# Kernel optimization log

Measured on AMD Instinct MI355X. Metric: run time of the kernel, lower is better.

## Reference

```python
import jax, jax.numpy as jnp
import numpy as np

B, TD, SD, H = 512, 2048, 768, 128


def setup_inputs() -> dict:
    key = jax.random.key(0)
    ks = jax.random.split(key, 12)
    s = lambda k, shape, fan_in: jax.random.normal(k, shape, jnp.float32) * (1.0 / np.sqrt(fan_in))
    return {
        "teacher_features": jax.random.normal(ks[0], (B, TD), jnp.float32),
        "student_features": jax.random.normal(ks[1], (B, SD), jnp.float32),
        # Linear weights stored [in, out] (transposed vs torch) so y = x @ W + b
        "Wt": s(ks[2], (TD, H), TD), "bt": jnp.zeros((H,), jnp.float32),
        "Ws": s(ks[3], (SD, H), SD), "bs": jnp.zeros((H,), jnp.float32),
        "W1": s(ks[4], (2 * H, H), 2 * H), "b1": jnp.zeros((H,), jnp.float32),
        "W2": s(ks[5], (H, 1), H), "b2": jnp.zeros((1,), jnp.float32),
    }


def reference(teacher_features, student_features, Wt, bt, Ws, bs, W1, b1, W2, b2):
    def compute_relations(f):
        b, h = f.shape
        # pairwise concat [f_i, f_j] -> [B, B, 2H]
        pair = jnp.concatenate(
            [jnp.broadcast_to(f[:, None, :], (b, b, h)),
             jnp.broadcast_to(f[None, :, :], (b, b, h))], axis=-1)
        hdn = jax.nn.relu(jnp.einsum('ijk,kh->ijh', pair, W1) + b1)
        rel = jax.nn.sigmoid(jnp.einsum('ijh,ho->ijo', hdn, W2) + b2)[..., 0]
        # diagonal stays zero (i != j in the original loop)
        return rel * (1.0 - jnp.eye(b, dtype=rel.dtype))

    tp = teacher_features @ Wt + bt  # [B, H]
    sp = student_features @ Ws + bs  # [B, H]
    t_rel = compute_relations(tp)
    s_rel = compute_relations(sp)
    return jnp.mean((s_rel - t_rel) ** 2)
```

## Files before the change

### kernel.cpp

```cpp
#include <hip/hip_runtime.h>

#define HDIM 128
#define BDIM 512

typedef __attribute__((ext_vector_type(8))) __bf16 bf16x8;
typedef __attribute__((ext_vector_type(4))) float  f32x4;
typedef __attribute__((ext_vector_type(2))) float  f32x2;

template<int K>
__device__ __forceinline__ f32x4 proj_acc(const float* __restrict__ F,
                                          const float* __restrict__ W,
                                          int m0, int n0, int wv, int l)
{
    constexpr int Ks = K >> 2;
    const int q = l >> 4, ln = l & 15;
    const float* Fp = &F[(size_t)(m0 + ln) * K + wv * Ks + q * 8];
    const float* Wp = &W[(size_t)(wv * Ks + q * 8) * HDIM + n0 + ln];
    f32x4 acc = {0.f, 0.f, 0.f, 0.f};
    #pragma unroll
    for (int k0 = 0; k0 < Ks; k0 += 32) {
        const float4 fa0 = *(const float4*)(Fp + k0);
        const float4 fa1 = *(const float4*)(Fp + k0 + 4);
        bf16x8 a, b;
        a[0] = (__bf16)fa0.x; a[1] = (__bf16)fa0.y; a[2] = (__bf16)fa0.z; a[3] = (__bf16)fa0.w;
        a[4] = (__bf16)fa1.x; a[5] = (__bf16)fa1.y; a[6] = (__bf16)fa1.z; a[7] = (__bf16)fa1.w;
        #pragma unroll
        for (int j = 0; j < 8; ++j)
            b[j] = (__bf16)Wp[(size_t)(k0 + j) * HDIM];
        acc = __builtin_amdgcn_mfma_f32_16x16x32_bf16(a, b, acc, 0, 0, 0);
    }
    return acc;
}

__global__ __launch_bounds__(256) void proj_mfma(
    const float* __restrict__ Ft, const float* __restrict__ Fs,
    const float* __restrict__ Wt, const float* __restrict__ Ws,
    __bf16* __restrict__ Pbt, __bf16* __restrict__ Pbs)
{
    const int tid = threadIdx.x;
    const int wv = tid >> 6, l = tid & 63;

    const int bid = blockIdx.x;
    const int c  = bid & 7;
    const int tt = bid >> 3;
    const int ntile = tt & 7;
    const int g  = ((tt >> 3) << 3) + c;
    const int net = g >> 5, mtile = g & 31;

    const int m0 = mtile * 16, n0 = ntile * 16;

    f32x4 acc;
    __bf16* P;
    if (net == 0) { acc = proj_acc<2048>(Ft, Wt, m0, n0, wv, l); P = Pbt; }
    else          { acc = proj_acc<768 >(Fs, Ws, m0, n0, wv, l); P = Pbs; }

    __shared__ float lds[4 * 256];
    #pragma unroll
    for (int r = 0; r < 4; ++r) lds[wv * 256 + r * 64 + l] = acc[r];
    __syncthreads();

    {
        const float s = lds[tid] + lds[256 + tid] + lds[512 + tid] + lds[768 + tid];
        const int r = tid >> 6, l2 = tid & 63;
        const int row = m0 + ((l2 >> 4) << 2) + r;
        const int col = n0 + (l2 & 15);
        P[(size_t)row * HDIM + col] = (__bf16)s;
    }
}

__global__ __launch_bounds__(64) void uv_mfma(
    const __bf16* __restrict__ Pbt, const __bf16* __restrict__ Pbs,
    const float* __restrict__ bt, const float* __restrict__ bs,
    const float* __restrict__ W1, const float* __restrict__ b1,
    __bf16* __restrict__ Ut, __bf16* __restrict__ Vt,
    __bf16* __restrict__ Us, __bf16* __restrict__ Vs,
    float* __restrict__ out)
{
    const int t = blockIdx.x;
    const int net = t >> 9, uvh = (t >> 8) & 1;
    const int mtile = (t >> 3) & 31, ntile = t & 7;
    const int l = threadIdx.x;

    if (t == 0 && l == 0) out[0] = 0.f;

    const __bf16* P   = net ? Pbs : Pbt;
    const float* bias = net ? bs : bt;
    __bf16* O = net ? (uvh ? Vs : Us) : (uvh ? Vt : Ut);
    const float* W1o = W1 + (size_t)uvh * HDIM * HDIM;

    const int m0 = mtile * 16, n0 = ntile * 16;
    const int q = l >> 4, ln = l & 15;
    const int arow = m0 + ln, bn = n0 + ln;

    f32x4 acc = {0.f, 0.f, 0.f, 0.f};
    float cpart = 0.f;
    #pragma unroll
    for (int k0 = 0; k0 < HDIM; k0 += 32) {
        const int ka = k0 + q * 8;
        bf16x8 a = *(const bf16x8*)&P[(size_t)arow * HDIM + ka];
        bf16x8 b;
        #pragma unroll
        for (int j = 0; j < 8; ++j) {
            const float w = W1o[(size_t)(ka + j) * HDIM + bn];
            b[j] = (__bf16)w;
            cpart = fmaf(bias[ka + j], w, cpart);
        }
        acc = __builtin_amdgcn_mfma_f32_16x16x32_bf16(a, b, acc, 0, 0, 0);
    }
    cpart += __shfl_xor(cpart, 16, 64);
    cpart += __shfl_xor(cpart, 32, 64);
    const float cfull = cpart + (uvh == 0 ? b1[bn] : 0.f);

    #pragma unroll
    for (int r = 0; r < 4; ++r) {
        const int row = m0 + q * 4 + r;
        O[(size_t)row * HDIM + bn] = (__bf16)(acc[r] + cfull);
    }
}

__device__ __forceinline__ f32x2 bfpair(unsigned d) {
    f32x2 r;
    r.x = __uint_as_float(d << 16);
    r.y = __uint_as_float(d & 0xffff0000u);
    return r;
}

#define PAIR_STEP(DU0,DU1,DV0,DV1,DP0,DP1,DQ0,DQ1,WK)                         \
    {                                                                          \
        const f32x2 u0_ = bfpair(DU0), u1_ = bfpair(DU1);                      \
        const f32x2 v0_ = bfpair(DV0), v1_ = bfpair(DV1);                      \
        const f32x2 p0_ = bfpair(DP0), p1_ = bfpair(DP1);                      \
        const f32x2 q0_ = bfpair(DQ0), q1_ = bfpair(DQ1);                      \
        aT00 = __builtin_elementwise_fma(__builtin_elementwise_max(u0_+v0_,z2), WK, aT00); \
        aT01 = __builtin_elementwise_fma(__builtin_elementwise_max(u0_+v1_,z2), WK, aT01); \
        aT10 = __builtin_elementwise_fma(__builtin_elementwise_max(u1_+v0_,z2), WK, aT10); \
        aT11 = __builtin_elementwise_fma(__builtin_elementwise_max(u1_+v1_,z2), WK, aT11); \
        aS00 = __builtin_elementwise_fma(__builtin_elementwise_max(p0_+q0_,z2), WK, aS00); \
        aS01 = __builtin_elementwise_fma(__builtin_elementwise_max(p0_+q1_,z2), WK, aS01); \
        aS10 = __builtin_elementwise_fma(__builtin_elementwise_max(p1_+q0_,z2), WK, aS10); \
        aS11 = __builtin_elementwise_fma(__builtin_elementwise_max(p1_+q1_,z2), WK, aS11); \
    }

__global__ __launch_bounds__(256, 4) void pair_kernel(
    const __bf16* __restrict__ Ut, const __bf16* __restrict__ Vt,
    const __bf16* __restrict__ Us, const __bf16* __restrict__ Vs,
    const float* __restrict__ W2, const float* __restrict__ b2,
    float* __restrict__ out)
{
    __shared__ alignas(16) unsigned short tU[32 * 136];
    __shared__ alignas(16) unsigned short tV[32 * 136];
    __shared__ alignas(16) unsigned short tP[32 * 136];
    __shared__ alignas(16) unsigned short tQ[32 * 136];
    __shared__ float red[256];

    const int tx = threadIdx.x, ty = threadIdx.y;
    const int tid = ty * 16 + tx;
    const int i0 = blockIdx.y * 32, j0 = blockIdx.x * 32;

    #pragma unroll
    for (int it = 0; it < 2; ++it) {
        const int s = tid + it * 256;
        const int r = s >> 4, c8 = s & 15;
        *(uint4*)&tU[r * 136 + c8 * 8] = *(const uint4*)&Ut[(size_t)(i0 + r) * HDIM + c8 * 8];
        *(uint4*)&tV[r * 136 + c8 * 8] = *(const uint4*)&Vt[(size_t)(j0 + r) * HDIM + c8 * 8];
        *(uint4*)&tP[r * 136 + c8 * 8] = *(const uint4*)&Us[(size_t)(i0 + r) * HDIM + c8 * 8];
        *(uint4*)&tQ[r * 136 + c8 * 8] = *(const uint4*)&Vs[(size_t)(j0 + r) * HDIM + c8 * 8];
    }
    __syncthreads();

    f32x2 aT00 = {0.f,0.f}, aT01 = {0.f,0.f}, aT10 = {0.f,0.f}, aT11 = {0.f,0.f};
    f32x2 aS00 = {0.f,0.f}, aS01 = {0.f,0.f}, aS10 = {0.f,0.f}, aS11 = {0.f,0.f};
    const f32x2 z2 = {0.f, 0.f};
    const float4* W24 = (const float4*)W2;

    #pragma unroll 2
    for (int h8 = 0; h8 < 16; ++h8) {
        const float4 wA = W24[h8 * 2 + 0];
        const float4 wB = W24[h8 * 2 + 1];
        const f32x2 w0 = {wA.x, wA.y}, w1 = {wA.z, wA.w};
        const f32x2 w2 = {wB.x, wB.y}, w3 = {wB.z, wB.w};

        const uint4 du0 = *(const uint4*)&tU[(ty     ) * 136 + h8 * 8];
        const uint4 du1 = *(const uint4*)&tU[(ty + 16) * 136 + h8 * 8];
        const uint4 dv0 = *(const uint4*)&tV[(tx     ) * 136 + h8 * 8];
        const uint4 dv1 = *(const uint4*)&tV[(tx + 16) * 136 + h8 * 8];
        const uint4 dp0 = *(const uint4*)&tP[(ty     ) * 136 + h8 * 8];
        const uint4 dp1 = *(const uint4*)&tP[(ty + 16) * 136 + h8 * 8];
        const uint4 dq0 = *(const uint4*)&tQ[(tx     ) * 136 + h8 * 8];
        const uint4 dq1 = *(const uint4*)&tQ[(tx + 16) * 136 + h8 * 8];

        PAIR_STEP(du0.x, du1.x, dv0.x, dv1.x, dp0.x, dp1.x, dq0.x, dq1.x, w0)
        PAIR_STEP(du0.y, du1.y, dv0.y, dv1.y, dp0.y, dp1.y, dq0.y, dq1.y, w1)
        PAIR_STEP(du0.z, du1.z, dv0.z, dv1.z, dp0.z, dp1.z, dq0.z, dq1.z, w2)
        PAIR_STEP(du0.w, du1.w, dv0.w, dv1.w, dp0.w, dp1.w, dq0.w, dq1.w, w3)
    }

    const float b2v = b2[0];
    float local = 0.f;
    {
        const float sT[2][2] = {{aT00.x + aT00.y, aT01.x + aT01.y},
                                {aT10.x + aT10.y, aT11.x + aT11.y}};
        const float sS[2][2] = {{aS00.x + aS00.y, aS01.x + aS01.y},
                                {aS10.x + aS10.y, aS11.x + aS11.y}};
        #pragma unroll
        for (int a = 0; a < 2; ++a)
            #pragma unroll
            for (int b = 0; b < 2; ++b) {
                const int i = i0 + ty + 16 * a;
                const int j = j0 + tx + 16 * b;
                if (i != j) {
                    const float tr = 1.f / (1.f + __expf(-(sT[a][b] + b2v)));
                    const float sr = 1.f / (1.f + __expf(-(sS[a][b] + b2v)));
                    const float d = sr - tr;
                    local = fmaf(d, d, local);
                }
            }
    }

    red[tid] = local;
    __syncthreads();
    #pragma unroll
    for (int s = 128; s > 0; s >>= 1) {
        if (tid < s) red[tid] += red[tid + s];
        __syncthreads();
    }
    if (tid == 0)
        atomicAdd(out, red[0] * (1.0f / ((float)BDIM * (float)BDIM)));
}

extern "C" void kernel_launch(void* const* d_in, const int* in_sizes, int n_in,
                              void* d_out, int out_size, void* d_ws, size_t ws_size,
                              hipStream_t stream) {
    const float* teacher = (const float*)d_in[0];
    const float* student = (const float*)d_in[1];
    const float* Wt = (const float*)d_in[2];
    const float* bt = (const float*)d_in[3];
    const float* Ws = (const float*)d_in[4];
    const float* bs = (const float*)d_in[5];
    const float* W1 = (const float*)d_in[6];
    const float* b1 = (const float*)d_in[7];
    const float* W2 = (const float*)d_in[8];
    const float* b2 = (const float*)d_in[9];
    float* out = (float*)d_out;

    const size_t M = (size_t)BDIM * HDIM;
    __bf16* Pbt = (__bf16*)d_ws;
    __bf16* Pbs = Pbt + M;
    __bf16* Ut = Pbs + M;
    __bf16* Vt = Ut + M;
    __bf16* Us = Vt + M;
    __bf16* Vs = Us + M;

    proj_mfma<<<512, 256, 0, stream>>>(teacher, student, Wt, Ws, Pbt, Pbs);

    uv_mfma<<<1024, 64, 0, stream>>>(Pbt, Pbs, bt, bs, W1, b1,
                                     Ut, Vt, Us, Vs, out);

    pair_kernel<<<dim3(16, 16), dim3(16, 16), 0, stream>>>(
        Ut, Vt, Us, Vs, W2, b2, out);
}
```

Before: 95.84 us.

## Pre-pack weights into bf16 MFMA fragment layout in a prep kernel

Adds a prep kernel that converts Wt, Ws and W1 from fp32 into bf16 laid out in the MFMA B-fragment order, and precomputes the bias-folded constant vector once. The projection and UV kernels then read each B fragment with a single 16-byte load instead of eight strided fp32 loads plus conversions, and the per-block bias dot product is removed. This costs an extra kernel launch and extra workspace traffic each call, and the launch count rises from three to four.

```diff
diff --git a/kernel.cpp b/kernel.cpp
--- a/kernel.cpp
+++ b/kernel.cpp
@@ -7,34 +7,89 @@
 typedef __attribute__((ext_vector_type(4))) float  f32x4;
 typedef __attribute__((ext_vector_type(2))) float  f32x2;
 
+__global__ __launch_bounds__(256) void prep_kernel(
+    const float* __restrict__ Wt, const float* __restrict__ Ws,
+    const float* __restrict__ W1, const float* __restrict__ b1,
+    const float* __restrict__ bt, const float* __restrict__ bs,
+    __bf16* __restrict__ WtF, __bf16* __restrict__ WsF,
+    __bf16* __restrict__ W1F, float* __restrict__ cvec,
+    float* __restrict__ out)
+{
+    const int b = blockIdx.x, t = threadIdx.x;
+    if (b < 128) {
+        const int g = b * 256 + t;
+        const int l = g & 63, e = g >> 6;
+        const int ks = e & 63, ntile = e >> 6;
+        const int q = l >> 4, ln = l & 15;
+        const float* src = &Wt[(size_t)(ks * 32 + q * 8) * HDIM + ntile * 16 + ln];
+        bf16x8 v;
+        #pragma unroll
+        for (int j = 0; j < 8; ++j) v[j] = (__bf16)src[j * HDIM];
+        *(bf16x8*)&WtF[(size_t)g * 8] = v;
+    } else if (b < 176) {
+        const int g = (b - 128) * 256 + t;
+        const int l = g & 63, e = g >> 6;
+        const int ks = e % 24, ntile = e / 24;
+        const int q = l >> 4, ln = l & 15;
+        const float* src = &Ws[(size_t)(ks * 32 + q * 8) * HDIM + ntile * 16 + ln];
+        bf16x8 v;
+        #pragma unroll
+        for (int j = 0; j < 8; ++j) v[j] = (__bf16)src[j * HDIM];
+        *(bf16x8*)&WsF[(size_t)g * 8] = v;
+    } else if (b < 192) {
+        const int g = (b - 176) * 256 + t;
+        const int l = g & 63, e = g >> 6;
+        const int ks = e & 3, nt = (e >> 2) & 7, uvh = e >> 5;
+        const int q = l >> 4, ln = l & 15;
+        const float* src = &W1[(size_t)uvh * HDIM * HDIM
+                               + (size_t)(ks * 32 + q * 8) * HDIM + nt * 16 + ln];
+        bf16x8 v;
+        #pragma unroll
+        for (int j = 0; j < 8; ++j) v[j] = (__bf16)src[j * HDIM];
+        *(bf16x8*)&W1F[(size_t)g * 8] = v;
+    } else {
+        if (t == 0) out[0] = 0.f;
+        #pragma unroll
+        for (int it = 0; it < 2; ++it) {
+            const int s = it * 256 + t;
+            const int net = s >> 8, uvh = (s >> 7) & 1, n = s & 127;
+            const float* bias = net ? bs : bt;
+            const float* Wc = W1 + (size_t)uvh * HDIM * HDIM + n;
+            float c = (uvh == 0) ? b1[n] : 0.f;
+            for (int k = 0; k < HDIM; ++k)
+                c = fmaf(bias[k], Wc[(size_t)k * HDIM], c);
+            cvec[s] = c;
+        }
+    }
+}
+
 template<int K>
 __device__ __forceinline__ f32x4 proj_acc(const float* __restrict__ F,
-                                          const float* __restrict__ W,
-                                          int m0, int n0, int wv, int l)
+                                          const __bf16* __restrict__ WF,
+                                          int m0, int ntile, int wv, int l)
 {
     constexpr int Ks = K >> 2;
+    constexpr int KS = K >> 5;
     const int q = l >> 4, ln = l & 15;
     const float* Fp = &F[(size_t)(m0 + ln) * K + wv * Ks + q * 8];
-    const float* Wp = &W[(size_t)(wv * Ks + q * 8) * HDIM + n0 + ln];
+    const __bf16* Wp = &WF[(size_t)((ntile * KS + (wv * Ks >> 5)) * 64 + l) * 8];
     f32x4 acc = {0.f, 0.f, 0.f, 0.f};
     #pragma unroll
     for (int k0 = 0; k0 < Ks; k0 += 32) {
         const float4 fa0 = *(const float4*)(Fp + k0);
         const float4 fa1 = *(const float4*)(Fp + k0 + 4);
-        bf16x8 a, b;
+        bf16x8 a;
         a[0] = (__bf16)fa0.x; a[1] = (__bf16)fa0.y; a[2] = (__bf16)fa0.z; a[3] = (__bf16)fa0.w;
         a[4] = (__bf16)fa1.x; a[5] = (__bf16)fa1.y; a[6] = (__bf16)fa1.z; a[7] = (__bf16)fa1.w;
-        #pragma unroll
-        for (int j = 0; j < 8; ++j)
-            b[j] = (__bf16)Wp[(size_t)(k0 + j) * HDIM];
-        acc = __builtin_amdgcn_mfma_f32_16x16x32_bf16(a, b, acc, 0, 0, 0);
+        const bf16x8 bfr = *(const bf16x8*)(Wp + (size_t)(k0 >> 5) * 64 * 8);
+        acc = __builtin_amdgcn_mfma_f32_16x16x32_bf16(a, bfr, acc, 0, 0, 0);
     }
     return acc;
 }
 
 __global__ __launch_bounds__(256) void proj_mfma(
     const float* __restrict__ Ft, const float* __restrict__ Fs,
-    const float* __restrict__ Wt, const float* __restrict__ Ws,
+    const __bf16* __restrict__ WtF, const __bf16* __restrict__ WsF,
     __bf16* __restrict__ Pbt, __bf16* __restrict__ Pbs)
 {
     const int tid = threadIdx.x;
@@ -51,8 +106,8 @@
 
     f32x4 acc;
     __bf16* P;
-    if (net == 0) { acc = proj_acc<2048>(Ft, Wt, m0, n0, wv, l); P = Pbt; }
-    else          { acc = proj_acc<768 >(Fs, Ws, m0, n0, wv, l); P = Pbs; }
+    if (net == 0) { acc = proj_acc<2048>(Ft, WtF, m0, ntile, wv, l); P = Pbt; }
+    else          { acc = proj_acc<768 >(Fs, WsF, m0, ntile, wv, l); P = Pbs; }
 
     __shared__ float lds[4 * 256];
     #pragma unroll
@@ -70,46 +125,32 @@
 
 __global__ __launch_bounds__(64) void uv_mfma(
     const __bf16* __restrict__ Pbt, const __bf16* __restrict__ Pbs,
-    const float* __restrict__ bt, const float* __restrict__ bs,
-    const float* __restrict__ W1, const float* __restrict__ b1,
+    const __bf16* __restrict__ W1F, const float* __restrict__ cvec,
     __bf16* __restrict__ Ut, __bf16* __restrict__ Vt,
-    __bf16* __restrict__ Us, __bf16* __restrict__ Vs,
-    float* __restrict__ out)
+    __bf16* __restrict__ Us, __bf16* __restrict__ Vs)
 {
     const int t = blockIdx.x;
     const int net = t >> 9, uvh = (t >> 8) & 1;
     const int mtile = (t >> 3) & 31, ntile = t & 7;
     const int l = threadIdx.x;
 
-    if (t == 0 && l == 0) out[0] = 0.f;
-
-    const __bf16* P   = net ? Pbs : Pbt;
-    const float* bias = net ? bs : bt;
+    const __bf16* P = net ? Pbs : Pbt;
     __bf16* O = net ? (uvh ? Vs : Us) : (uvh ? Vt : Ut);
-    const float* W1o = W1 + (size_t)uvh * HDIM * HDIM;
 
     const int m0 = mtile * 16, n0 = ntile * 16;
     const int q = l >> 4, ln = l & 15;
     const int arow = m0 + ln, bn = n0 + ln;
 
+    const __bf16* Wp = &W1F[(size_t)(((uvh * 8 + ntile) * 4) * 64 + l) * 8];
+
     f32x4 acc = {0.f, 0.f, 0.f, 0.f};
-    float cpart = 0.f;
-    #pragma unroll
-    for (int k0 = 0; k0 < HDIM; k0 += 32) {
-        const int ka = k0 + q * 8;
-        bf16x8 a = *(const bf16x8*)&P[(size_t)arow * HDIM + ka];
-        bf16x8 b;
-        #pragma unroll
-        for (int j = 0; j < 8; ++j) {
-            const float w = W1o[(size_t)(ka + j) * HDIM + bn];
-            b[j] = (__bf16)w;
-            cpart = fmaf(bias[ka + j], w, cpart);
-        }
+    #pragma unroll
+    for (int ks = 0; ks < 4; ++ks) {
+        const bf16x8 a = *(const bf16x8*)&P[(size_t)arow * HDIM + ks * 32 + q * 8];
+        const bf16x8 b = *(const bf16x8*)(Wp + (size_t)ks * 64 * 8);
         acc = __builtin_amdgcn_mfma_f32_16x16x32_bf16(a, b, acc, 0, 0, 0);
     }
-    cpart += __shfl_xor(cpart, 16, 64);
-    cpart += __shfl_xor(cpart, 32, 64);
-    const float cfull = cpart + (uvh == 0 ? b1[bn] : 0.f);
+    const float cfull = cvec[((net * 2 + uvh) << 7) + bn];
 
     #pragma unroll
     for (int r = 0; r < 4; ++r) {
@@ -246,15 +287,22 @@
     const size_t M = (size_t)BDIM * HDIM;
     __bf16* Pbt = (__bf16*)d_ws;
     __bf16* Pbs = Pbt + M;
-    __bf16* Ut = Pbs + M;
-    __bf16* Vt = Ut + M;
-    __bf16* Us = Vt + M;
-    __bf16* Vs = Us + M;
-
-    proj_mfma<<<512, 256, 0, stream>>>(teacher, student, Wt, Ws, Pbt, Pbs);
-
-    uv_mfma<<<1024, 64, 0, stream>>>(Pbt, Pbs, bt, bs, W1, b1,
-                                     Ut, Vt, Us, Vs, out);
+    __bf16* Ut  = Pbs + M;
+    __bf16* Vt  = Ut + M;
+    __bf16* Us  = Vt + M;
+    __bf16* Vs  = Us + M;
+    __bf16* WtF = Vs + M;
+    __bf16* WsF = WtF + (size_t)32768 * 8;
+    __bf16* W1F = WsF + (size_t)12288 * 8;
+    float*  cvec = (float*)(W1F + (size_t)4096 * 8);
+
+    prep_kernel<<<193, 256, 0, stream>>>(Wt, Ws, W1, b1, bt, bs,
+                                         WtF, WsF, W1F, cvec, out);
+
+    proj_mfma<<<512, 256, 0, stream>>>(teacher, student, WtF, WsF, Pbt, Pbs);
+
+    uv_mfma<<<1024, 64, 0, stream>>>(Pbt, Pbs, W1F, cvec,
+                                     Ut, Vt, Us, Vs);
 
     pair_kernel<<<dim3(16, 16), dim3(16, 16), 0, stream>>>(
         Ut, Vt, Us, Vs, W2, b2, out);
```

New measurement: 105.5 us. 10.1% more time.

## Fuse projection, UV and pair stages into one cooperative kernel with grid syncs

Applied to the files above, without the earlier changes.

Merges the three kernels into a single cooperative launch of 512 blocks, using grid-wide syncs between the projection, U/V, and pairwise stages. The pair stage is re-tiled to 16x32 tiles so 512 blocks cover the grid, with each thread now computing two pairs instead of four. This removes two kernel launch gaps but adds grid barrier costs, idles half the waves in the UV stage, and requires all 512 blocks to be co-resident.

```diff
diff --git a/kernel.cpp b/kernel.cpp
--- a/kernel.cpp
+++ b/kernel.cpp
@@ -1,4 +1,7 @@
 #include <hip/hip_runtime.h>
+#include <hip/hip_cooperative_groups.h>
+
+namespace cg = cooperative_groups;
 
 #define HDIM 128
 #define BDIM 512
@@ -6,6 +9,7 @@
 typedef __attribute__((ext_vector_type(8))) __bf16 bf16x8;
 typedef __attribute__((ext_vector_type(4))) float  f32x4;
 typedef __attribute__((ext_vector_type(2))) float  f32x2;
+typedef unsigned short ushort_t;
 
 template<int K>
 __device__ __forceinline__ f32x4 proj_acc(const float* __restrict__ F,
@@ -32,92 +36,6 @@
     return acc;
 }
 
-__global__ __launch_bounds__(256) void proj_mfma(
-    const float* __restrict__ Ft, const float* __restrict__ Fs,
-    const float* __restrict__ Wt, const float* __restrict__ Ws,
-    __bf16* __restrict__ Pbt, __bf16* __restrict__ Pbs)
-{
-    const int tid = threadIdx.x;
-    const int wv = tid >> 6, l = tid & 63;
-
-    const int bid = blockIdx.x;
-    const int c  = bid & 7;
-    const int tt = bid >> 3;
-    const int ntile = tt & 7;
-    const int g  = ((tt >> 3) << 3) + c;
-    const int net = g >> 5, mtile = g & 31;
-
-    const int m0 = mtile * 16, n0 = ntile * 16;
-
-    f32x4 acc;
-    __bf16* P;
-    if (net == 0) { acc = proj_acc<2048>(Ft, Wt, m0, n0, wv, l); P = Pbt; }
-    else          { acc = proj_acc<768 >(Fs, Ws, m0, n0, wv, l); P = Pbs; }
-
-    __shared__ float lds[4 * 256];
-    #pragma unroll
-    for (int r = 0; r < 4; ++r) lds[wv * 256 + r * 64 + l] = acc[r];
-    __syncthreads();
-
-    {
-        const float s = lds[tid] + lds[256 + tid] + lds[512 + tid] + lds[768 + tid];
-        const int r = tid >> 6, l2 = tid & 63;
-        const int row = m0 + ((l2 >> 4) << 2) + r;
-        const int col = n0 + (l2 & 15);
-        P[(size_t)row * HDIM + col] = (__bf16)s;
-    }
-}
-
-__global__ __launch_bounds__(64) void uv_mfma(
-    const __bf16* __restrict__ Pbt, const __bf16* __restrict__ Pbs,
-    const float* __restrict__ bt, const float* __restrict__ bs,
-    const float* __restrict__ W1, const float* __restrict__ b1,
-    __bf16* __restrict__ Ut, __bf16* __restrict__ Vt,
-    __bf16* __restrict__ Us, __bf16* __restrict__ Vs,
-    float* __restrict__ out)
-{
-    const int t = blockIdx.x;
-    const int net = t >> 9, uvh = (t >> 8) & 1;
-    const int mtile = (t >> 3) & 31, ntile = t & 7;
-    const int l = threadIdx.x;
-
-    if (t == 0 && l == 0) out[0] = 0.f;
-
-    const __bf16* P   = net ? Pbs : Pbt;
-    const float* bias = net ? bs : bt;
-    __bf16* O = net ? (uvh ? Vs : Us) : (uvh ? Vt : Ut);
-    const float* W1o = W1 + (size_t)uvh * HDIM * HDIM;
-
-    const int m0 = mtile * 16, n0 = ntile * 16;
-    const int q = l >> 4, ln = l & 15;
-    const int arow = m0 + ln, bn = n0 + ln;
-
-    f32x4 acc = {0.f, 0.f, 0.f, 0.f};
-    float cpart = 0.f;
-    #pragma unroll
-    for (int k0 = 0; k0 < HDIM; k0 += 32) {
-        const int ka = k0 + q * 8;
-        bf16x8 a = *(const bf16x8*)&P[(size_t)arow * HDIM + ka];
-        bf16x8 b;
-        #pragma unroll
-        for (int j = 0; j < 8; ++j) {
-            const float w = W1o[(size_t)(ka + j) * HDIM + bn];
-            b[j] = (__bf16)w;
-            cpart = fmaf(bias[ka + j], w, cpart);
-        }
-        acc = __builtin_amdgcn_mfma_f32_16x16x32_bf16(a, b, acc, 0, 0, 0);
-    }
-    cpart += __shfl_xor(cpart, 16, 64);
-    cpart += __shfl_xor(cpart, 32, 64);
-    const float cfull = cpart + (uvh == 0 ? b1[bn] : 0.f);
-
-    #pragma unroll
-    for (int r = 0; r < 4; ++r) {
-        const int row = m0 + q * 4 + r;
-        O[(size_t)row * HDIM + bn] = (__bf16)(acc[r] + cfull);
-    }
-}
-
 __device__ __forceinline__ f32x2 bfpair(unsigned d) {
     f32x2 r;
     r.x = __uint_as_float(d << 16);
@@ -125,107 +43,186 @@
     return r;
 }
 
-#define PAIR_STEP(DU0,DU1,DV0,DV1,DP0,DP1,DQ0,DQ1,WK)                         \
+#define PSTEP(DU,DV0,DV1,DP,DQ0,DQ1,WK)                                        \
     {                                                                          \
-        const f32x2 u0_ = bfpair(DU0), u1_ = bfpair(DU1);                      \
+        const f32x2 u_  = bfpair(DU);                                          \
         const f32x2 v0_ = bfpair(DV0), v1_ = bfpair(DV1);                      \
-        const f32x2 p0_ = bfpair(DP0), p1_ = bfpair(DP1);                      \
+        const f32x2 p_  = bfpair(DP);                                          \
         const f32x2 q0_ = bfpair(DQ0), q1_ = bfpair(DQ1);                      \
-        aT00 = __builtin_elementwise_fma(__builtin_elementwise_max(u0_+v0_,z2), WK, aT00); \
-        aT01 = __builtin_elementwise_fma(__builtin_elementwise_max(u0_+v1_,z2), WK, aT01); \
-        aT10 = __builtin_elementwise_fma(__builtin_elementwise_max(u1_+v0_,z2), WK, aT10); \
-        aT11 = __builtin_elementwise_fma(__builtin_elementwise_max(u1_+v1_,z2), WK, aT11); \
-        aS00 = __builtin_elementwise_fma(__builtin_elementwise_max(p0_+q0_,z2), WK, aS00); \
-        aS01 = __builtin_elementwise_fma(__builtin_elementwise_max(p0_+q1_,z2), WK, aS01); \
-        aS10 = __builtin_elementwise_fma(__builtin_elementwise_max(p1_+q0_,z2), WK, aS10); \
-        aS11 = __builtin_elementwise_fma(__builtin_elementwise_max(p1_+q1_,z2), WK, aS11); \
-    }
-
-__global__ __launch_bounds__(256, 4) void pair_kernel(
-    const __bf16* __restrict__ Ut, const __bf16* __restrict__ Vt,
-    const __bf16* __restrict__ Us, const __bf16* __restrict__ Vs,
+        aT0 = __builtin_elementwise_fma(__builtin_elementwise_max(u_+v0_,z2), WK, aT0); \
+        aT1 = __builtin_elementwise_fma(__builtin_elementwise_max(u_+v1_,z2), WK, aT1); \
+        aS0 = __builtin_elementwise_fma(__builtin_elementwise_max(p_+q0_,z2), WK, aS0); \
+        aS1 = __builtin_elementwise_fma(__builtin_elementwise_max(p_+q1_,z2), WK, aS1); \
+    }
+
+__global__ __launch_bounds__(256, 2) void fused_kernel(
+    const float* __restrict__ Ft, const float* __restrict__ Fs,
+    const float* __restrict__ Wt, const float* __restrict__ Ws,
+    const float* __restrict__ bt, const float* __restrict__ bs,
+    const float* __restrict__ W1, const float* __restrict__ b1,
     const float* __restrict__ W2, const float* __restrict__ b2,
+    __bf16* __restrict__ Pbt, __bf16* __restrict__ Pbs,
+    __bf16* __restrict__ Ut, __bf16* __restrict__ Vt,
+    __bf16* __restrict__ Us, __bf16* __restrict__ Vs,
     float* __restrict__ out)
 {
-    __shared__ alignas(16) unsigned short tU[32 * 136];
-    __shared__ alignas(16) unsigned short tV[32 * 136];
-    __shared__ alignas(16) unsigned short tP[32 * 136];
-    __shared__ alignas(16) unsigned short tQ[32 * 136];
-    __shared__ float red[256];
-
-    const int tx = threadIdx.x, ty = threadIdx.y;
-    const int tid = ty * 16 + tx;
-    const int i0 = blockIdx.y * 32, j0 = blockIdx.x * 32;
-
-    #pragma unroll
-    for (int it = 0; it < 2; ++it) {
-        const int s = tid + it * 256;
-        const int r = s >> 4, c8 = s & 15;
-        *(uint4*)&tU[r * 136 + c8 * 8] = *(const uint4*)&Ut[(size_t)(i0 + r) * HDIM + c8 * 8];
-        *(uint4*)&tV[r * 136 + c8 * 8] = *(const uint4*)&Vt[(size_t)(j0 + r) * HDIM + c8 * 8];
-        *(uint4*)&tP[r * 136 + c8 * 8] = *(const uint4*)&Us[(size_t)(i0 + r) * HDIM + c8 * 8];
-        *(uint4*)&tQ[r * 136 + c8 * 8] = *(const uint4*)&Vs[(size_t)(j0 + r) * HDIM + c8 * 8];
-    }
-    __syncthreads();
-
-    f32x2 aT00 = {0.f,0.f}, aT01 = {0.f,0.f}, aT10 = {0.f,0.f}, aT11 = {0.f,0.f};
-    f32x2 aS00 = {0.f,0.f}, aS01 = {0.f,0.f}, aS10 = {0.f,0.f}, aS11 = {0.f,0.f};
-    const f32x2 z2 = {0.f, 0.f};
-    const float4* W24 = (const float4*)W2;
-
-    #pragma unroll 2
-    for (int h8 = 0; h8 < 16; ++h8) {
-        const float4 wA = W24[h8 * 2 + 0];
-        const float4 wB = W24[h8 * 2 + 1];
-        const f32x2 w0 = {wA.x, wA.y}, w1 = {wA.z, wA.w};
-        const f32x2 w2 = {wB.x, wB.y}, w3 = {wB.z, wB.w};
-
-        const uint4 du0 = *(const uint4*)&tU[(ty     ) * 136 + h8 * 8];
-        const uint4 du1 = *(const uint4*)&tU[(ty + 16) * 136 + h8 * 8];
-        const uint4 dv0 = *(const uint4*)&tV[(tx     ) * 136 + h8 * 8];
-        const uint4 dv1 = *(const uint4*)&tV[(tx + 16) * 136 + h8 * 8];
-        const uint4 dp0 = *(const uint4*)&tP[(ty     ) * 136 + h8 * 8];
-        const uint4 dp1 = *(const uint4*)&tP[(ty + 16) * 136 + h8 * 8];
-        const uint4 dq0 = *(const uint4*)&tQ[(tx     ) * 136 + h8 * 8];
-        const uint4 dq1 = *(const uint4*)&tQ[(tx + 16) * 136 + h8 * 8];
-
-        PAIR_STEP(du0.x, du1.x, dv0.x, dv1.x, dp0.x, dp1.x, dq0.x, dq1.x, w0)
-        PAIR_STEP(du0.y, du1.y, dv0.y, dv1.y, dp0.y, dp1.y, dq0.y, dq1.y, w1)
-        PAIR_STEP(du0.z, du1.z, dv0.z, dv1.z, dp0.z, dp1.z, dq0.z, dq1.z, w2)
-        PAIR_STEP(du0.w, du1.w, dv0.w, dv1.w, dp0.w, dp1.w, dq0.w, dq1.w, w3)
-    }
-
-    const float b2v = b2[0];
-    float local = 0.f;
+    __shared__ __align__(16) char smem[27136];
+
+    cg::grid_group grid = cg::this_grid();
+    const int tid = threadIdx.x;
+    const int bid = blockIdx.x;
+    const int wv = tid >> 6, l = tid & 63;
+
+    if (bid == 0 && tid == 0) out[0] = 0.f;
+
     {
-        const float sT[2][2] = {{aT00.x + aT00.y, aT01.x + aT01.y},
-                                {aT10.x + aT10.y, aT11.x + aT11.y}};
-        const float sS[2][2] = {{aS00.x + aS00.y, aS01.x + aS01.y},
-                                {aS10.x + aS10.y, aS11.x + aS11.y}};
-        #pragma unroll
-        for (int a = 0; a < 2; ++a)
+        float* lds = (float*)smem;
+        const int c  = bid & 7;
+        const int tt = bid >> 3;
+        const int ntile = tt & 7;
+        const int g  = ((tt >> 3) << 3) + c;
+        const int net = g >> 5, mtile = g & 31;
+        const int m0 = mtile * 16, n0 = ntile * 16;
+
+        f32x4 acc;
+        __bf16* P;
+        if (net == 0) { acc = proj_acc<2048>(Ft, Wt, m0, n0, wv, l); P = Pbt; }
+        else          { acc = proj_acc<768 >(Fs, Ws, m0, n0, wv, l); P = Pbs; }
+
+        #pragma unroll
+        for (int r = 0; r < 4; ++r) lds[wv * 256 + r * 64 + l] = acc[r];
+        __syncthreads();
+        {
+            const float s = lds[tid] + lds[256 + tid] + lds[512 + tid] + lds[768 + tid];
+            const int r = tid >> 6, l2 = tid & 63;
+            const int row = m0 + ((l2 >> 4) << 2) + r;
+            const int col = n0 + (l2 & 15);
+            P[(size_t)row * HDIM + col] = (__bf16)s;
+        }
+    }
+
+    grid.sync();
+
+    if (wv < 2) {
+        const int t = bid * 2 + wv;
+        const int net = t >> 9, uvh = (t >> 8) & 1;
+        const int mtile = (t >> 3) & 31, ntile = t & 7;
+
+        const __bf16* P   = net ? Pbs : Pbt;
+        const float* bias = net ? bs : bt;
+        __bf16* O = net ? (uvh ? Vs : Us) : (uvh ? Vt : Ut);
+        const float* W1o = W1 + (size_t)uvh * HDIM * HDIM;
+
+        const int m0 = mtile * 16, n0 = ntile * 16;
+        const int q = l >> 4, ln = l & 15;
+        const int arow = m0 + ln, bn = n0 + ln;
+
+        f32x4 acc = {0.f, 0.f, 0.f, 0.f};
+        float cpart = 0.f;
+        #pragma unroll
+        for (int k0 = 0; k0 < HDIM; k0 += 32) {
+            const int ka = k0 + q * 8;
+            bf16x8 a = *(const bf16x8*)&P[(size_t)arow * HDIM + ka];
+            bf16x8 b;
+            #pragma unroll
+            for (int j = 0; j < 8; ++j) {
+                const float w = W1o[(size_t)(ka + j) * HDIM + bn];
+                b[j] = (__bf16)w;
+                cpart = fmaf(bias[ka + j], w, cpart);
+            }
+            acc = __builtin_amdgcn_mfma_f32_16x16x32_bf16(a, b, acc, 0, 0, 0);
+        }
+        cpart += __shfl_xor(cpart, 16, 64);
+        cpart += __shfl_xor(cpart, 32, 64);
+        const float cfull = cpart + (uvh == 0 ? b1[bn] : 0.f);
+
+        #pragma unroll
+        for (int r = 0; r < 4; ++r) {
+            const int row = m0 + q * 4 + r;
+            O[(size_t)row * HDIM + bn] = (__bf16)(acc[r] + cfull);
+        }
+    }
+
+    grid.sync();
+
+    {
+        ushort_t* tU = (ushort_t*)smem;
+        ushort_t* tP = tU + 16 * 136;
+        ushort_t* tV = tP + 16 * 136;
+        ushort_t* tQ = tV + 32 * 136;
+        float*   red = (float*)(smem + 26112);
+
+        const int tx = tid & 15, ty = tid >> 4;
+        const int it = bid >> 4, jt = bid & 15;
+        const int i0 = it * 16, j0 = jt * 32;
+
+        {
+            const int r = tid >> 4, c8 = tid & 15;
+            *(uint4*)&tU[r * 136 + c8 * 8] = *(const uint4*)&Ut[(size_t)(i0 + r) * HDIM + c8 * 8];
+            *(uint4*)&tP[r * 136 + c8 * 8] = *(const uint4*)&Us[(size_t)(i0 + r) * HDIM + c8 * 8];
+            #pragma unroll
+            for (int it2 = 0; it2 < 2; ++it2) {
+                const int s = tid + it2 * 256;
+                const int rr = s >> 4, cc = s & 15;
+                *(uint4*)&tV[rr * 136 + cc * 8] = *(const uint4*)&Vt[(size_t)(j0 + rr) * HDIM + cc * 8];
+                *(uint4*)&tQ[rr * 136 + cc * 8] = *(const uint4*)&Vs[(size_t)(j0 + rr) * HDIM + cc * 8];
+            }
+        }
+        __syncthreads();
+
+        f32x2 aT0 = {0.f,0.f}, aT1 = {0.f,0.f};
+        f32x2 aS0 = {0.f,0.f}, aS1 = {0.f,0.f};
+        const f32x2 z2 = {0.f, 0.f};
+        const float4* W24 = (const float4*)W2;
+
+        #pragma unroll 2
+        for (int h8 = 0; h8 < 16; ++h8) {
+            const float4 wA = W24[h8 * 2 + 0];
+            const float4 wB = W24[h8 * 2 + 1];
+            const f32x2 w0 = {wA.x, wA.y}, w1 = {wA.z, wA.w};
+            const f32x2 w2 = {wB.x, wB.y}, w3 = {wB.z, wB.w};
+
+            const uint4 du  = *(const uint4*)&tU[(ty     ) * 136 + h8 * 8];
+            const uint4 dp  = *(const uint4*)&tP[(ty     ) * 136 + h8 * 8];
+            const uint4 dv0 = *(const uint4*)&tV[(tx     ) * 136 + h8 * 8];
+            const uint4 dv1 = *(const uint4*)&tV[(tx + 16) * 136 + h8 * 8];
+            const uint4 dq0 = *(const uint4*)&tQ[(tx     ) * 136 + h8 * 8];
+            const uint4 dq1 = *(const uint4*)&tQ[(tx + 16) * 136 + h8 * 8];
+
+            PSTEP(du.x, dv0.x, dv1.x, dp.x, dq0.x, dq1.x, w0)
+            PSTEP(du.y, dv0.y, dv1.y, dp.y, dq0.y, dq1.y, w1)
+            PSTEP(du.z, dv0.z, dv1.z, dp.z, dq0.z, dq1.z, w2)
+            PSTEP(du.w, dv0.w, dv1.w, dp.w, dq0.w, dq1.w, w3)
+        }
+
+        const float b2v = b2[0];
+        float local = 0.f;
+        {
+            const float sT[2] = {aT0.x + aT0.y, aT1.x + aT1.y};
+            const float sS[2] = {aS0.x + aS0.y, aS1.x + aS1.y};
             #pragma unroll
             for (int b = 0; b < 2; ++b) {
-                const int i = i0 + ty + 16 * a;
+                const int i = i0 + ty;
                 const int j = j0 + tx + 16 * b;
                 if (i != j) {
-                    const float tr = 1.f / (1.f + __expf(-(sT[a][b] + b2v)));
-                    const float sr = 1.f / (1.f + __expf(-(sS[a][b] + b2v)));
+                    const float tr = 1.f / (1.f + __expf(-(sT[b] + b2v)));
+                    const float sr = 1.f / (1.f + __expf(-(sS[b] + b2v)));
                     const float d = sr - tr;
                     local = fmaf(d, d, local);
                 }
             }
-    }
-
-    red[tid] = local;
-    __syncthreads();
-    #pragma unroll
-    for (int s = 128; s > 0; s >>= 1) {
-        if (tid < s) red[tid] += red[tid + s];
+        }
+
+        red[tid] = local;
         __syncthreads();
-    }
-    if (tid == 0)
-        atomicAdd(out, red[0] * (1.0f / ((float)BDIM * (float)BDIM)));
+        #pragma unroll
+        for (int s = 128; s > 0; s >>= 1) {
+            if (tid < s) red[tid] += red[tid + s];
+            __syncthreads();
+        }
+        if (tid == 0)
+            atomicAdd(out, red[0] * (1.0f / ((float)BDIM * (float)BDIM)));
+    }
 }
 
 extern "C" void kernel_launch(void* const* d_in, const int* in_sizes, int n_in,
@@ -246,16 +243,20 @@
     const size_t M = (size_t)BDIM * HDIM;
     __bf16* Pbt = (__bf16*)d_ws;
     __bf16* Pbs = Pbt + M;
-    __bf16* Ut = Pbs + M;
-    __bf16* Vt = Ut + M;
-    __bf16* Us = Vt + M;
-    __bf16* Vs = Us + M;
-
-    proj_mfma<<<512, 256, 0, stream>>>(teacher, student, Wt, Ws, Pbt, Pbs);
-
-    uv_mfma<<<1024, 64, 0, stream>>>(Pbt, Pbs, bt, bs, W1, b1,
-                                     Ut, Vt, Us, Vs, out);
-
-    pair_kernel<<<dim3(16, 16), dim3(16, 16), 0, stream>>>(
-        Ut, Vt, Us, Vs, W2, b2, out);
-}
+    __bf16* Ut  = Pbs + M;
+    __bf16* Vt  = Ut + M;
+    __bf16* Us  = Vt + M;
+    __bf16* Vs  = Us + M;
+
+    void* args[] = {
+        (void*)&teacher, (void*)&student,
+        (void*)&Wt, (void*)&Ws, (void*)&bt, (void*)&bs,
+        (void*)&W1, (void*)&b1, (void*)&W2, (void*)&b2,
+        (void*)&Pbt, (void*)&Pbs,
+        (void*)&Ut, (void*)&Vt, (void*)&Us, (void*)&Vs,
+        (void*)&out
+    };
+
+    hipLaunchCooperativeKernel((void*)fused_kernel, dim3(512), dim3(256),
+                               args, 0, stream);
+}
```

Measured after the change: 223.4 us. +133.1%, slower.
